# Kernel tuning notes

Hardware: AMD Instinct MI355X
Metric: run time of the kernel (lower is better)

The kernel has to match this reference:

```python
import jax, jax.numpy as jnp
import numpy as np

NUM_HEADS = 8

def setup_inputs() -> dict:
    key0 = jax.random.key(0)
    ks = jax.random.split(key0, 6)
    T, S, B, E = 2048, 2048, 2, 256
    W_SCALE = 0.06  # ~xavier_uniform std for 256x256
    return {
        "query": jax.random.normal(ks[0], (T, B, E), dtype=jnp.float32),
        "key": jax.random.normal(ks[1], (S, B, E), dtype=jnp.float32),
        "value": jax.random.normal(ks[2], (S, B, E), dtype=jnp.float32),
        "Wq": jax.random.normal(ks[3], (E, E), dtype=jnp.float32) * W_SCALE,
        "bq": jnp.zeros((E,), dtype=jnp.float32),
        "Wk": jax.random.normal(ks[4], (E, E), dtype=jnp.float32) * W_SCALE,
        "bk": jnp.zeros((E,), dtype=jnp.float32),
        "Wo": jax.random.normal(ks[5], (E, E), dtype=jnp.float32) * W_SCALE,
        "bo": jnp.zeros((E,), dtype=jnp.float32),
    }

def reference(query, key, value, Wq, bq, Wk, bk, Wo, bo):
    # query: [T,B,E], key/value: [S,B,E]
    T, B, E = query.shape
    S = key.shape[0]
    H = NUM_HEADS
    Dh = E // H
    q = jnp.einsum('tbe,fe->tbf', query, Wq) + bq
    k = jnp.einsum('sbe,fe->sbf', key, Wk) + bk
    # split heads: view(L, B*H, Dh) == reshape(L, B, H, Dh)
    qh = q.reshape(T, B, H, Dh)
    kh = k.reshape(S, B, H, Dh)
    vh = value.reshape(S, B, H, Dh)  # v is NOT projected in this module
    scale = 1.0 / jnp.sqrt(jnp.asarray(Dh, dtype=query.dtype))
    scores = jnp.einsum('tbhd,sbhd->bhts', qh * scale, kh)  # [B,H,T,S]
    attn = jax.nn.softmax(scores, axis=-1)
    out = jnp.einsum('bhts,sbhd->tbhd', attn, vh).reshape(T, B, E)
    # residual output projection: out + linear(out)
    out = out + jnp.einsum('tbe,fe->tbf', out, Wo) + bo
    avg_weights = jnp.mean(attn, axis=1)  # [B,T,S]
    return (out, avg_weights)
```

## Files before the change

### kernel.cpp

```cpp
#include <hip/hip_runtime.h>
#include <hip/hip_fp16.h>

#define T_DIM 2048
#define S_DIM 2048
#define B_DIM 2
#define E_DIM 256
#define H_DIM 8
#define DH 32

typedef _Float16 half8 __attribute__((ext_vector_type(8)));
typedef _Float16 half4 __attribute__((ext_vector_type(4)));
typedef float floatx4 __attribute__((ext_vector_type(4)));

#if defined(__has_builtin)
#if __has_builtin(__builtin_amdgcn_exp2f)
#define EXPFN(x) __builtin_amdgcn_exp2f(x)
#define LOG2E_FOLD 1.4426950408889634f
#endif
#endif
#ifndef EXPFN
#define EXPFN(x) __expf(x)
#define LOG2E_FOLD 1.0f
#endif

__global__ __launch_bounds__(256) void prep_kernel(const float* __restrict__ V,
                                                   _Float16* __restrict__ Vt2,
                                                   const float* __restrict__ Wq,
                                                   const float* __restrict__ Wk,
                                                   const float* __restrict__ Wo,
                                                   _Float16* __restrict__ Wqh,
                                                   _Float16* __restrict__ Wkh,
                                                   _Float16* __restrict__ Woh) {
  __shared__ float tile[64][33];
  int tid = threadIdx.x;
  int bx = blockIdx.x;
  if (bx < 512) {
    int st = bx & 31, h = (bx >> 5) & 7, b = bx >> 8;
    int s0 = st * 64;
    int d = tid & 31, sr = tid >> 5;
#pragma unroll
    for (int k = 0; k < 8; ++k) {
      int s = sr + k * 8;
      tile[s][d] = V[((size_t)(s0 + s) * B_DIM + b) * E_DIM + h * DH + d];
    }
    __syncthreads();
    int si = tid & 63, dq = tid >> 6;
    size_t base = ((size_t)b * H_DIM + h) * 128 * 512;
    int tl = st * 4 + (si >> 4);
    int sl = si & 15;
#pragma unroll
    for (int m = 0; m < 8; ++m) {
      int dd = dq * 8 + m;
      Vt2[base + (size_t)tl * 512 + dd * 16 + sl] = (_Float16)tile[si][dd];
    }
  } else {
    int i = (bx - 512) * 2048 + tid * 8;
    int sel = i >> 16, off = i & 65535;
    const float* src = sel == 0 ? Wq : (sel == 1 ? Wk : Wo);
    _Float16* dst = sel == 0 ? Wqh : (sel == 1 ? Wkh : Woh);
    float4 a0 = *(const float4*)(src + off);
    float4 a1 = *(const float4*)(src + off + 4);
    half8 hv;
    hv[0]=(_Float16)a0.x; hv[1]=(_Float16)a0.y; hv[2]=(_Float16)a0.z; hv[3]=(_Float16)a0.w;
    hv[4]=(_Float16)a1.x; hv[5]=(_Float16)a1.y; hv[6]=(_Float16)a1.z; hv[7]=(_Float16)a1.w;
    if (sel == 2) {
      int f = off >> 8, e0 = off & 255;
      int di = f - e0;
      if (di >= 0 && di < 8) hv[di] += (_Float16)1.0f;
    }
    *(half8*)(dst + off) = hv;
  }
}

#define XS 264
__global__ __launch_bounds__(256, 4) void proj_mfma(const float* __restrict__ Q,
                                                    const float* __restrict__ K,
                                                    const _Float16* __restrict__ Wqh,
                                                    const _Float16* __restrict__ Wkh,
                                                    const float* __restrict__ bq,
                                                    const float* __restrict__ bk,
                                                    _Float16* __restrict__ Qp,
                                                    _Float16* __restrict__ Kp,
                                                    float scale_q) {
  __shared__ _Float16 Xs[64 * XS];
  int z = blockIdx.z;
  const float* X = z ? K : Q;
  const _Float16* Wh = z ? Wkh : Wqh;
  const float* bias = z ? bk : bq;
  _Float16* out = z ? Kp : Qp;
  float scale = z ? 1.0f : scale_q;

  int tid = threadIdx.x;
  int lane = tid & 63, w = tid >> 6;
  int quad = lane >> 4, l16 = lane & 15;
  int r0 = blockIdx.x * 64;
  int c0 = blockIdx.y * 64;

#pragma unroll
  for (int it = 0; it < 16; ++it) {
    int row = (tid >> 6) + it * 4, col = (tid & 63) * 4;
    float4 a = *(const float4*)(X + (size_t)(r0 + row) * 256 + col);
    half4 hv;
    hv[0] = (_Float16)a.x; hv[1] = (_Float16)a.y;
    hv[2] = (_Float16)a.z; hv[3] = (_Float16)a.w;
    *(half4*)(Xs + row * XS + col) = hv;
  }
  __syncthreads();

  floatx4 c[4] = {{0.f,0.f,0.f,0.f},{0.f,0.f,0.f,0.f},{0.f,0.f,0.f,0.f},{0.f,0.f,0.f,0.f}};
  int arow = w * 16 + l16;
#pragma unroll
  for (int k0 = 0; k0 < 256; k0 += 32) {
    half8 af = *(const half8*)(Xs + arow * XS + k0 + quad * 8);
#pragma unroll
    for (int j = 0; j < 4; ++j) {
      int f = c0 + j * 16 + l16;
      half8 bf = *(const half8*)(Wh + (size_t)f * 256 + k0 + quad * 8);
      c[j] = __builtin_amdgcn_mfma_f32_16x16x32_f16(af, bf, c[j], 0, 0, 0);
    }
  }
#pragma unroll
  for (int j = 0; j < 4; ++j) {
    int f = c0 + j * 16 + l16;
    float bv = bias[f];
    int h = f >> 5, d = f & 31;
#pragma unroll
    for (int r = 0; r < 4; ++r) {
      int row = r0 + w * 16 + quad * 4 + r;
      int t = row >> 1, b = row & 1;
      out[(((size_t)b * H_DIM + h) * T_DIM + t) * DH + d] =
          (_Float16)((c[j][r] + bv) * scale);
    }
  }
}

#define OSTRIDE 36
__global__ __launch_bounds__(512, 2) void attn_o_kernel(const _Float16* __restrict__ Qp,
                                                        const _Float16* __restrict__ Kp,
                                                        const _Float16* __restrict__ Vt2,
                                                        _Float16* __restrict__ Of16,
                                                        float* __restrict__ lsum) {
  __shared__ float stageO[8][64 * OSTRIDE];
  __shared__ float lstage[8][64];

  int tid = threadIdx.x;
  int lane = tid & 63, w = tid >> 6;
  int quad = lane >> 4, l16 = lane & 15;
  int bx = blockIdx.x;
  int h = bx & 7, b = (bx >> 3) & 1, tcc = bx >> 4;
  int t0 = tcc << 6;

  const _Float16* Qb = Qp + (((size_t)b * H_DIM + h) * T_DIM + t0) * DH;
  const _Float16* Kb = Kp + ((size_t)b * H_DIM + h) * S_DIM * DH;
  const _Float16* Vb = Vt2 + ((size_t)b * H_DIM + h) * 128 * 512;

  half8 qf[4];
#pragma unroll
  for (int j = 0; j < 4; ++j)
    qf[j] = *(const half8*)(Qb + (size_t)(j * 16 + l16) * DH + quad * 8);

  floatx4 o[4][2];
#pragma unroll
  for (int j = 0; j < 4; ++j) { o[j][0] = (floatx4){0,0,0,0}; o[j][1] = (floatx4){0,0,0,0}; }
  float ls[4] = {0.f, 0.f, 0.f, 0.f};

  int tile0 = w * 16;
  half8 kf[2];
  half4 v0[2], v1[2];
  kf[0] = *(const half8*)(Kb + (size_t)(tile0 * 16 + l16) * DH + quad * 8);
  v0[0] = *(const half4*)(Vb + (size_t)tile0 * 512 + l16 * 16 + quad * 4);
  v1[0] = *(const half4*)(Vb + (size_t)tile0 * 512 + 256 + l16 * 16 + quad * 4);

#pragma unroll
  for (int i = 0; i < 16; ++i) {
    int cur = i & 1, nxt = cur ^ 1;
    if (i < 15) {
      int tl = tile0 + i + 1;
      kf[nxt] = *(const half8*)(Kb + (size_t)(tl * 16 + l16) * DH + quad * 8);
      v0[nxt] = *(const half4*)(Vb + (size_t)tl * 512 + l16 * 16 + quad * 4);
      v1[nxt] = *(const half4*)(Vb + (size_t)tl * 512 + 256 + l16 * 16 + quad * 4);
    }
#pragma unroll
    for (int j = 0; j < 4; ++j) {
      floatx4 c = {0.f, 0.f, 0.f, 0.f};
      c = __builtin_amdgcn_mfma_f32_16x16x32_f16(kf[cur], qf[j], c, 0, 0, 0);
      float e0 = EXPFN(c[0]), e1 = EXPFN(c[1]), e2 = EXPFN(c[2]), e3 = EXPFN(c[3]);
      ls[j] += (e0 + e1) + (e2 + e3);
      half4 p;
      p[0] = (_Float16)e0; p[1] = (_Float16)e1; p[2] = (_Float16)e2; p[3] = (_Float16)e3;
      o[j][0] = __builtin_amdgcn_mfma_f32_16x16x16f16(p, v0[cur], o[j][0], 0, 0, 0);
      o[j][1] = __builtin_amdgcn_mfma_f32_16x16x16f16(p, v1[cur], o[j][1], 0, 0, 0);
    }
  }

#pragma unroll
  for (int j = 0; j < 4; ++j) {
    float v = ls[j];
    v += __shfl_xor(v, 16, 64);
    v += __shfl_xor(v, 32, 64);
    if (quad == 0) lstage[w][j * 16 + l16] = v;
  }
#pragma unroll
  for (int j = 0; j < 4; ++j)
#pragma unroll
    for (int r = 0; r < 4; ++r) {
      stageO[w][(j * 16 + quad * 4 + r) * OSTRIDE + l16] = o[j][0][r];
      stageO[w][(j * 16 + quad * 4 + r) * OSTRIDE + 16 + l16] = o[j][1][r];
    }
  __syncthreads();

  int t = tid >> 3, d0 = (tid & 7) * 4;
  floatx4 os = {0.f, 0.f, 0.f, 0.f};
  float lr = 0.f;
#pragma unroll
  for (int ww = 0; ww < 8; ++ww) {
    os += *(const floatx4*)&stageO[ww][t * OSTRIDE + d0];
    lr += lstage[ww][t];
  }
  float rl = 1.0f / lr;
  half4 oh;
  oh[0] = (_Float16)(os[0] * rl); oh[1] = (_Float16)(os[1] * rl);
  oh[2] = (_Float16)(os[2] * rl); oh[3] = (_Float16)(os[3] * rl);
  *(half4*)(Of16 + ((size_t)(t0 + t) * B_DIM + b) * E_DIM + h * DH + d0) = oh;
  if (tid < 64) {
    float s = 0.f;
#pragma unroll
    for (int ww = 0; ww < 8; ++ww) s += lstage[ww][tid];
    lsum[((size_t)b * H_DIM + h) * T_DIM + t0 + tid] = s;
  }
}

#define ASTRIDE 132
__global__ __launch_bounds__(512, 2) void avg_kernel(const _Float16* __restrict__ Qp,
                                                     const _Float16* __restrict__ Kp,
                                                     const float* __restrict__ lsum,
                                                     float* __restrict__ avg_out) {
  __shared__ float ldsA[128 * ASTRIDE];

  int tid = threadIdx.x;
  int lane = tid & 63, w = tid >> 6;
  int quad = lane >> 4, l16 = lane & 15;
  int bx = blockIdx.x;
  int sc = bx & 15, tc = (bx >> 4) & 15, b = bx >> 8;
  int t0 = tc * 128, s0 = sc * 128;
  int tw = t0 + w * 16;

  floatx4 acc[8];
#pragma unroll
  for (int st = 0; st < 8; ++st) acc[st] = (floatx4){0.f, 0.f, 0.f, 0.f};

  for (int h = 0; h < H_DIM; ++h) {
    const _Float16* Qb = Qp + (((size_t)b * H_DIM + h) * T_DIM + tw) * DH;
    const _Float16* Kb = Kp + (((size_t)b * H_DIM + h) * S_DIM + s0) * DH;
    half8 qfrag = *(const half8*)(Qb + (size_t)l16 * DH + quad * 8);
    float rlv = 0.125f / lsum[((size_t)b * H_DIM + h) * T_DIM + tw + l16];
#pragma unroll
    for (int st = 0; st < 8; ++st) {
      half8 kf = *(const half8*)(Kb + (size_t)(st * 16 + l16) * DH + quad * 8);
      floatx4 c = {0.f, 0.f, 0.f, 0.f};
      c = __builtin_amdgcn_mfma_f32_16x16x32_f16(kf, qfrag, c, 0, 0, 0);
#pragma unroll
      for (int r = 0; r < 4; ++r) acc[st][r] += EXPFN(c[r]) * rlv;
    }
  }
#pragma unroll
  for (int st = 0; st < 8; ++st)
    *(floatx4*)&ldsA[(w * 16 + l16) * ASTRIDE + st * 16 + quad * 4] = acc[st];
  __syncthreads();

  int rbase = tid >> 4, seg = tid & 15;
#pragma unroll
  for (int rr = 0; rr < 4; ++rr) {
    int row = rr * 32 + rbase;
    const float* srcl = &ldsA[row * ASTRIDE];
    float* dst = avg_out + ((size_t)b * T_DIM + t0 + row) * S_DIM + s0;
#pragma unroll
    for (int k = 0; k < 2; ++k) {
      int col = seg * 4 + k * 64;
      *(floatx4*)(dst + col) = *(const floatx4*)(srcl + col);
    }
  }
}

__global__ __launch_bounds__(256, 4) void outproj_mfma(const _Float16* __restrict__ Of16,
                                                       const _Float16* __restrict__ Woh,
                                                       const float* __restrict__ bo,
                                                       float* __restrict__ out) {
  __shared__ _Float16 Os[64 * XS];
  int tid = threadIdx.x;
  int lane = tid & 63, w = tid >> 6;
  int quad = lane >> 4, l16 = lane & 15;
  int r0 = blockIdx.x * 64;
  int c0 = blockIdx.y * 64;

#pragma unroll
  for (int it = 0; it < 8; ++it) {
    int row = (tid >> 5) + it * 8, col = (tid & 31) * 8;
    *(half8*)(Os + row * XS + col) =
        *(const half8*)(Of16 + (size_t)(r0 + row) * 256 + col);
  }
  __syncthreads();

  floatx4 c[4] = {{0.f,0.f,0.f,0.f},{0.f,0.f,0.f,0.f},{0.f,0.f,0.f,0.f},{0.f,0.f,0.f,0.f}};
  int arow = w * 16 + l16;
#pragma unroll
  for (int k0 = 0; k0 < 256; k0 += 32) {
    half8 af = *(const half8*)(Os + arow * XS + k0 + quad * 8);
#pragma unroll
    for (int j = 0; j < 4; ++j) {
      int f = c0 + j * 16 + l16;
      half8 bf = *(const half8*)(Woh + (size_t)f * 256 + k0 + quad * 8);
      c[j] = __builtin_amdgcn_mfma_f32_16x16x32_f16(af, bf, c[j], 0, 0, 0);
    }
  }
#pragma unroll
  for (int j = 0; j < 4; ++j) {
    int f = c0 + j * 16 + l16;
    float bv = bo[f];
#pragma unroll
    for (int r = 0; r < 4; ++r) {
      int row = r0 + w * 16 + quad * 4 + r;
      out[(size_t)row * 256 + f] = c[j][r] + bv;
    }
  }
}

extern "C" void kernel_launch(void* const* d_in, const int* in_sizes, int n_in,
                              void* d_out, int out_size, void* d_ws, size_t ws_size,
                              hipStream_t stream) {
  const float* query = (const float*)d_in[0];
  const float* key   = (const float*)d_in[1];
  const float* value = (const float*)d_in[2];
  const float* Wq    = (const float*)d_in[3];
  const float* bq    = (const float*)d_in[4];
  const float* Wk    = (const float*)d_in[5];
  const float* bk    = (const float*)d_in[6];
  const float* Wo    = (const float*)d_in[7];
  const float* bo    = (const float*)d_in[8];

  float* out = (float*)d_out;
  float* avg_out = out + (size_t)T_DIM * B_DIM * E_DIM;

  char* ws = (char*)d_ws;
  _Float16* Qp   = (_Float16*)ws;
  _Float16* Kp   = (_Float16*)(ws + (2u << 20));
  _Float16* Vt2  = (_Float16*)(ws + (4u << 20));
  _Float16* Of16 = (_Float16*)(ws + (6u << 20));
  float*    lsum = (float*)(ws + (8u << 20));
  _Float16* Wqh  = (_Float16*)(ws + (8u << 20) + (128u << 10));
  _Float16* Wkh  = (_Float16*)(ws + (8u << 20) + (256u << 10));
  _Float16* Woh  = (_Float16*)(ws + (8u << 20) + (384u << 10));

  const float scale_q = 0.17677669529663687f * LOG2E_FOLD;

  prep_kernel<<<dim3(608), dim3(256), 0, stream>>>(value, Vt2, Wq, Wk, Wo, Wqh, Wkh, Woh);
  proj_mfma<<<dim3(64, 4, 2), dim3(256), 0, stream>>>(query, key, Wqh, Wkh, bq, bk,
                                                      Qp, Kp, scale_q);
  attn_o_kernel<<<dim3(512), dim3(512), 0, stream>>>(Qp, Kp, Vt2, Of16, lsum);
  avg_kernel<<<dim3(512), dim3(512), 0, stream>>>(Qp, Kp, lsum, avg_out);
  outproj_mfma<<<dim3(64, 4), dim3(256), 0, stream>>>(Of16, Woh, bo, out);
}
```

Baseline: 140.7 us.

## Fuse attention output and head-averaged weights into one kernel

Merges attn_o_kernel and avg_kernel into a single kernel. Each block handles 16 query rows across all heads, keeps the fp16 probabilities in registers and accumulates the averaged weights after normalising by the row sum exchanged through double-buffered LDS. This removes the second QK^T matmul and exp pass, along with the lsum round trip through global memory. In exchange it uses only 256 blocks of 1024 threads, syncs once per head, and accumulates the averages in fp16, which loses precision.

```diff
diff --git a/kernel.cpp b/kernel.cpp
--- a/kernel.cpp
+++ b/kernel.cpp
@@ -135,150 +135,104 @@
 }
 
 #define OSTRIDE 36
-__global__ __launch_bounds__(512, 2) void attn_o_kernel(const _Float16* __restrict__ Qp,
-                                                        const _Float16* __restrict__ Kp,
-                                                        const _Float16* __restrict__ Vt2,
-                                                        _Float16* __restrict__ Of16,
-                                                        float* __restrict__ lsum) {
-  __shared__ float stageO[8][64 * OSTRIDE];
-  __shared__ float lstage[8][64];
+__global__ __launch_bounds__(1024, 4) void attn_fused(const _Float16* __restrict__ Qp,
+                                                      const _Float16* __restrict__ Kp,
+                                                      const _Float16* __restrict__ Vt2,
+                                                      _Float16* __restrict__ Of16,
+                                                      float* __restrict__ avg_out) {
+  __shared__ float stageO[2][16][16 * OSTRIDE];
+  __shared__ float lstage[2][16][16];
 
   int tid = threadIdx.x;
   int lane = tid & 63, w = tid >> 6;
   int quad = lane >> 4, l16 = lane & 15;
   int bx = blockIdx.x;
-  int h = bx & 7, b = (bx >> 3) & 1, tcc = bx >> 4;
-  int t0 = tcc << 6;
-
-  const _Float16* Qb = Qp + (((size_t)b * H_DIM + h) * T_DIM + t0) * DH;
-  const _Float16* Kb = Kp + ((size_t)b * H_DIM + h) * S_DIM * DH;
-  const _Float16* Vb = Vt2 + ((size_t)b * H_DIM + h) * 128 * 512;
-
-  half8 qf[4];
-#pragma unroll
-  for (int j = 0; j < 4; ++j)
-    qf[j] = *(const half8*)(Qb + (size_t)(j * 16 + l16) * DH + quad * 8);
-
-  floatx4 o[4][2];
-#pragma unroll
-  for (int j = 0; j < 4; ++j) { o[j][0] = (floatx4){0,0,0,0}; o[j][1] = (floatx4){0,0,0,0}; }
-  float ls[4] = {0.f, 0.f, 0.f, 0.f};
-
-  int tile0 = w * 16;
-  half8 kf[2];
-  half4 v0[2], v1[2];
-  kf[0] = *(const half8*)(Kb + (size_t)(tile0 * 16 + l16) * DH + quad * 8);
-  v0[0] = *(const half4*)(Vb + (size_t)tile0 * 512 + l16 * 16 + quad * 4);
-  v1[0] = *(const half4*)(Vb + (size_t)tile0 * 512 + 256 + l16 * 16 + quad * 4);
-
-#pragma unroll
-  for (int i = 0; i < 16; ++i) {
-    int cur = i & 1, nxt = cur ^ 1;
-    if (i < 15) {
-      int tl = tile0 + i + 1;
-      kf[nxt] = *(const half8*)(Kb + (size_t)(tl * 16 + l16) * DH + quad * 8);
-      v0[nxt] = *(const half4*)(Vb + (size_t)tl * 512 + l16 * 16 + quad * 4);
-      v1[nxt] = *(const half4*)(Vb + (size_t)tl * 512 + 256 + l16 * 16 + quad * 4);
-    }
-#pragma unroll
-    for (int j = 0; j < 4; ++j) {
+  int b = bx & 1, tc = bx >> 1;
+  int t0 = tc << 4;
+  int sbase = w << 7;
+  int tl0 = w << 3;
+
+  half4 avg_acc[8];
+#pragma unroll
+  for (int st = 0; st < 8; ++st) avg_acc[st] = (half4){0, 0, 0, 0};
+
+  for (int h = 0; h < H_DIM; ++h) {
+    const _Float16* Qb = Qp + (((size_t)b * H_DIM + h) * T_DIM + t0) * DH;
+    const _Float16* Kb = Kp + ((size_t)b * H_DIM + h) * S_DIM * DH;
+    const _Float16* Vb = Vt2 + ((size_t)b * H_DIM + h) * 128 * 512;
+
+    half8 qfrag = *(const half8*)(Qb + (size_t)l16 * DH + quad * 8);
+    floatx4 o0 = {0.f,0.f,0.f,0.f}, o1 = {0.f,0.f,0.f,0.f};
+    float lacc = 0.f;
+    half4 pst[8];
+
+    half8 kf[2];
+    half4 v0[2], v1[2];
+    kf[0] = *(const half8*)(Kb + (size_t)(sbase + l16) * DH + quad * 8);
+    v0[0] = *(const half4*)(Vb + (size_t)tl0 * 512 + l16 * 16 + quad * 4);
+    v1[0] = *(const half4*)(Vb + (size_t)tl0 * 512 + 256 + l16 * 16 + quad * 4);
+
+#pragma unroll
+    for (int st = 0; st < 8; ++st) {
+      int cur = st & 1, nxt = cur ^ 1;
+      if (st < 7) {
+        int tl = tl0 + st + 1;
+        kf[nxt] = *(const half8*)(Kb + (size_t)(tl * 16 + l16) * DH + quad * 8);
+        v0[nxt] = *(const half4*)(Vb + (size_t)tl * 512 + l16 * 16 + quad * 4);
+        v1[nxt] = *(const half4*)(Vb + (size_t)tl * 512 + 256 + l16 * 16 + quad * 4);
+      }
       floatx4 c = {0.f, 0.f, 0.f, 0.f};
-      c = __builtin_amdgcn_mfma_f32_16x16x32_f16(kf[cur], qf[j], c, 0, 0, 0);
+      c = __builtin_amdgcn_mfma_f32_16x16x32_f16(kf[cur], qfrag, c, 0, 0, 0);
       float e0 = EXPFN(c[0]), e1 = EXPFN(c[1]), e2 = EXPFN(c[2]), e3 = EXPFN(c[3]);
-      ls[j] += (e0 + e1) + (e2 + e3);
+      lacc += (e0 + e1) + (e2 + e3);
       half4 p;
       p[0] = (_Float16)e0; p[1] = (_Float16)e1; p[2] = (_Float16)e2; p[3] = (_Float16)e3;
-      o[j][0] = __builtin_amdgcn_mfma_f32_16x16x16f16(p, v0[cur], o[j][0], 0, 0, 0);
-      o[j][1] = __builtin_amdgcn_mfma_f32_16x16x16f16(p, v1[cur], o[j][1], 0, 0, 0);
-    }
-  }
-
-#pragma unroll
-  for (int j = 0; j < 4; ++j) {
-    float v = ls[j];
-    v += __shfl_xor(v, 16, 64);
-    v += __shfl_xor(v, 32, 64);
-    if (quad == 0) lstage[w][j * 16 + l16] = v;
-  }
-#pragma unroll
-  for (int j = 0; j < 4; ++j)
+      pst[st] = p;
+      o0 = __builtin_amdgcn_mfma_f32_16x16x16f16(p, v0[cur], o0, 0, 0, 0);
+      o1 = __builtin_amdgcn_mfma_f32_16x16x16f16(p, v1[cur], o1, 0, 0, 0);
+    }
+
+    int bufi = h & 1;
+    lacc += __shfl_xor(lacc, 16, 64);
+    lacc += __shfl_xor(lacc, 32, 64);
+    if (quad == 0) lstage[bufi][w][l16] = lacc;
 #pragma unroll
     for (int r = 0; r < 4; ++r) {
-      stageO[w][(j * 16 + quad * 4 + r) * OSTRIDE + l16] = o[j][0][r];
-      stageO[w][(j * 16 + quad * 4 + r) * OSTRIDE + 16 + l16] = o[j][1][r];
-    }
-  __syncthreads();
-
-  int t = tid >> 3, d0 = (tid & 7) * 4;
-  floatx4 os = {0.f, 0.f, 0.f, 0.f};
-  float lr = 0.f;
-#pragma unroll
-  for (int ww = 0; ww < 8; ++ww) {
-    os += *(const floatx4*)&stageO[ww][t * OSTRIDE + d0];
-    lr += lstage[ww][t];
-  }
-  float rl = 1.0f / lr;
-  half4 oh;
-  oh[0] = (_Float16)(os[0] * rl); oh[1] = (_Float16)(os[1] * rl);
-  oh[2] = (_Float16)(os[2] * rl); oh[3] = (_Float16)(os[3] * rl);
-  *(half4*)(Of16 + ((size_t)(t0 + t) * B_DIM + b) * E_DIM + h * DH + d0) = oh;
-  if (tid < 64) {
-    float s = 0.f;
-#pragma unroll
-    for (int ww = 0; ww < 8; ++ww) s += lstage[ww][tid];
-    lsum[((size_t)b * H_DIM + h) * T_DIM + t0 + tid] = s;
-  }
-}
-
-#define ASTRIDE 132
-__global__ __launch_bounds__(512, 2) void avg_kernel(const _Float16* __restrict__ Qp,
-                                                     const _Float16* __restrict__ Kp,
-                                                     const float* __restrict__ lsum,
-                                                     float* __restrict__ avg_out) {
-  __shared__ float ldsA[128 * ASTRIDE];
-
-  int tid = threadIdx.x;
-  int lane = tid & 63, w = tid >> 6;
-  int quad = lane >> 4, l16 = lane & 15;
-  int bx = blockIdx.x;
-  int sc = bx & 15, tc = (bx >> 4) & 15, b = bx >> 8;
-  int t0 = tc * 128, s0 = sc * 128;
-  int tw = t0 + w * 16;
-
-  floatx4 acc[8];
-#pragma unroll
-  for (int st = 0; st < 8; ++st) acc[st] = (floatx4){0.f, 0.f, 0.f, 0.f};
-
-  for (int h = 0; h < H_DIM; ++h) {
-    const _Float16* Qb = Qp + (((size_t)b * H_DIM + h) * T_DIM + tw) * DH;
-    const _Float16* Kb = Kp + (((size_t)b * H_DIM + h) * S_DIM + s0) * DH;
-    half8 qfrag = *(const half8*)(Qb + (size_t)l16 * DH + quad * 8);
-    float rlv = 0.125f / lsum[((size_t)b * H_DIM + h) * T_DIM + tw + l16];
-#pragma unroll
-    for (int st = 0; st < 8; ++st) {
-      half8 kf = *(const half8*)(Kb + (size_t)(st * 16 + l16) * DH + quad * 8);
-      floatx4 c = {0.f, 0.f, 0.f, 0.f};
-      c = __builtin_amdgcn_mfma_f32_16x16x32_f16(kf, qfrag, c, 0, 0, 0);
-#pragma unroll
-      for (int r = 0; r < 4; ++r) acc[st][r] += EXPFN(c[r]) * rlv;
-    }
-  }
-#pragma unroll
-  for (int st = 0; st < 8; ++st)
-    *(floatx4*)&ldsA[(w * 16 + l16) * ASTRIDE + st * 16 + quad * 4] = acc[st];
-  __syncthreads();
-
-  int rbase = tid >> 4, seg = tid & 15;
-#pragma unroll
-  for (int rr = 0; rr < 4; ++rr) {
-    int row = rr * 32 + rbase;
-    const float* srcl = &ldsA[row * ASTRIDE];
-    float* dst = avg_out + ((size_t)b * T_DIM + t0 + row) * S_DIM + s0;
-#pragma unroll
-    for (int k = 0; k < 2; ++k) {
-      int col = seg * 4 + k * 64;
-      *(floatx4*)(dst + col) = *(const floatx4*)(srcl + col);
-    }
+      stageO[bufi][w][(quad * 4 + r) * OSTRIDE + l16] = o0[r];
+      stageO[bufi][w][(quad * 4 + r) * OSTRIDE + 16 + l16] = o1[r];
+    }
+    __syncthreads();
+
+    float lrow = 0.f;
+#pragma unroll
+    for (int ww = 0; ww < 16; ++ww) lrow += lstage[bufi][ww][l16];
+    _Float16 rlh = (_Float16)(1.0f / lrow);
+    half4 rv; rv[0] = rlh; rv[1] = rlh; rv[2] = rlh; rv[3] = rlh;
+#pragma unroll
+    for (int st = 0; st < 8; ++st) avg_acc[st] += pst[st] * rv;
+
+    if (tid < 512) {
+      int t = tid >> 5, d = tid & 31;
+      float osum = 0.f, lr = 0.f;
+#pragma unroll
+      for (int ww = 0; ww < 16; ++ww) {
+        osum += stageO[bufi][ww][t * OSTRIDE + d];
+        lr += lstage[bufi][ww][t];
+      }
+      Of16[((size_t)(t0 + t) * B_DIM + b) * E_DIM + h * DH + d] =
+          (_Float16)(osum / lr);
+    }
+  }
+
+  float* ao = avg_out + ((size_t)b * T_DIM + t0 + l16) * S_DIM + sbase + quad * 4;
+#pragma unroll
+  for (int st = 0; st < 8; ++st) {
+    float4 o;
+    o.x = (float)avg_acc[st][0] * 0.125f;
+    o.y = (float)avg_acc[st][1] * 0.125f;
+    o.z = (float)avg_acc[st][2] * 0.125f;
+    o.w = (float)avg_acc[st][3] * 0.125f;
+    *(float4*)(ao + st * 16) = o;
   }
 }
 
@@ -346,7 +300,6 @@
   _Float16* Kp   = (_Float16*)(ws + (2u << 20));
   _Float16* Vt2  = (_Float16*)(ws + (4u << 20));
   _Float16* Of16 = (_Float16*)(ws + (6u << 20));
-  float*    lsum = (float*)(ws + (8u << 20));
   _Float16* Wqh  = (_Float16*)(ws + (8u << 20) + (128u << 10));
   _Float16* Wkh  = (_Float16*)(ws + (8u << 20) + (256u << 10));
   _Float16* Woh  = (_Float16*)(ws + (8u << 20) + (384u << 10));
@@ -356,7 +309,6 @@
   prep_kernel<<<dim3(608), dim3(256), 0, stream>>>(value, Vt2, Wq, Wk, Wo, Wqh, Wkh, Woh);
   proj_mfma<<<dim3(64, 4, 2), dim3(256), 0, stream>>>(query, key, Wqh, Wkh, bq, bk,
                                                       Qp, Kp, scale_q);
-  attn_o_kernel<<<dim3(512), dim3(512), 0, stream>>>(Qp, Kp, Vt2, Of16, lsum);
-  avg_kernel<<<dim3(512), dim3(512), 0, stream>>>(Qp, Kp, lsum, avg_out);
+  attn_fused<<<dim3(256), dim3(1024), 0, stream>>>(Qp, Kp, Vt2, Of16, avg_out);
   outproj_mfma<<<dim3(64, 4), dim3(256), 0, stream>>>(Of16, Woh, bo, out);
 }
```

After: 146.7 us. 4.2% more time.
